# Kernel optimization log

Hardware: AMD Instinct MI355X
Metric: run time of the kernel (lower is better)

The kernel has to match this reference:

```python
import jax, jax.numpy as jnp
import numpy as np

N_NODES = 100000
N_EDGES = 1600000
N_GRAPHS = 1024
DIM_IN = 128
DIM_SF = 32
DIM_OUT = 8
EPS = 1e-5


def setup_inputs() -> dict:
    key = jax.random.key(0)
    ks = jax.random.split(key, 16)
    feat = jax.random.normal(ks[0], (N_NODES, DIM_IN), dtype=jnp.float32)
    self_feat = jax.random.normal(ks[1], (N_GRAPHS, DIM_SF), dtype=jnp.float32)
    src = jax.random.randint(ks[2], (N_EDGES,), 0, N_NODES)
    dst = jax.random.randint(ks[3], (N_EDGES,), 0, N_NODES)
    node2graph = jnp.sort(jax.random.randint(ks[4], (N_NODES,), 0, N_GRAPHS))

    def lin(k, din, dout):
        s = 1.0 / np.sqrt(din)
        kw, kb = jax.random.split(k)
        W = jax.random.uniform(kw, (din, dout), minval=-s, maxval=s, dtype=jnp.float32)
        b = jax.random.uniform(kb, (dout,), minval=-s, maxval=s, dtype=jnp.float32)
        return W, b

    W1, b1 = lin(ks[5], DIM_IN, 100)
    W2, b2 = lin(ks[6], 100, 20)
    Wf1, bf1 = lin(ks[7], 20 * DIM_SF, 128)
    Wf2, bf2 = lin(ks[8], 128, 32)
    Wf3, bf3 = lin(ks[9], 32, DIM_OUT)
    g1 = jnp.ones((128,), jnp.float32); be1 = jnp.zeros((128,), jnp.float32)
    g2 = jnp.ones((32,), jnp.float32); be2 = jnp.zeros((32,), jnp.float32)
    return dict(feat=feat, self_feat=self_feat, src=src, dst=dst,
                node2graph=node2graph, W1=W1, b1=b1, W2=W2, b2=b2,
                Wf1=Wf1, bf1=bf1, g1=g1, be1=be1,
                Wf2=Wf2, bf2=bf2, g2=g2, be2=be2, Wf3=Wf3, bf3=bf3)


def _gcn_layer(h, src, dst, W, b):
    # copy_u + mean reduce: segment-mean of source features onto destinations.
    n = h.shape[0]
    msum = jax.ops.segment_sum(h[src], dst, num_segments=n)        # [N, d]
    deg = jax.ops.segment_sum(jnp.ones((src.shape[0], 1), h.dtype), dst,
                              num_segments=n)                      # [N, 1]
    # DGL: nodes with no incoming messages keep their previous 'h'.
    agg = jnp.where(deg > 0, msum / jnp.maximum(deg, 1.0), h)
    return agg @ W + b


def _bn(x, gamma, beta):
    # BatchNorm1d in training mode: biased batch statistics.
    mu = jnp.mean(x, axis=0)
    var = jnp.mean((x - mu) ** 2, axis=0)
    return (x - mu) / jnp.sqrt(var + EPS) * gamma + beta


def reference(feat, self_feat, src, dst, node2graph,
              W1, b1, W2, b2, Wf1, bf1, g1, be1, Wf2, bf2, g2, be2, Wf3, bf3):
    h = jax.nn.relu(_gcn_layer(feat, src, dst, W1, b1))            # [N, 100]
    h = jax.nn.relu(_gcn_layer(h, src, dst, W2, b2))               # [N, 20]
    # dgl.mean_nodes: per-graph mean pooling
    hsum = jax.ops.segment_sum(h, node2graph, num_segments=N_GRAPHS)
    cnt = jax.ops.segment_sum(jnp.ones((h.shape[0], 1), h.dtype), node2graph,
                              num_segments=N_GRAPHS)
    hg = hsum / jnp.maximum(cnt, 1.0)                              # [G, 20]
    # Kronecker fusion: bmm(hg[:, :, None], self_feat[:, None, :])
    fused = (hg[:, :, None] * self_feat[:, None, :]).reshape(hg.shape[0], -1)
    out = jax.nn.relu(_bn(fused @ Wf1 + bf1, g1, be1))
    out = jax.nn.relu(_bn(out @ Wf2 + bf2, g2, be2))
    return out @ Wf3 + bf3                                         # [G, 8]
```

## Files before the change

kernel.cpp:

```cpp
#include <hip/hip_runtime.h>
#include <hip/hip_fp16.h>

#define N_NODES 100000
#define N_EDGES 1600000
#define N_GRAPHS 1024
#define DIM_IN 128
#define D1 100
#define D1P 128
#define D2 20
#define D2P 32
#define DIM_SF 32
#define DF1 128
#define DF2 32
#define DOUT 8
#define EPS 1e-5f
#define NPW 8

typedef _Float16 hh2 __attribute__((ext_vector_type(2)));

__device__ __forceinline__ void fdacc(unsigned u, float& lo, float& hi) {
  const hh2 MLO = {(_Float16)1.0f, (_Float16)0.0f};
  const hh2 MHI = {(_Float16)0.0f, (_Float16)1.0f};
  hh2 h = __builtin_bit_cast(hh2, u);
  lo = __builtin_amdgcn_fdot2(h, MLO, lo, false);
  hi = __builtin_amdgcn_fdot2(h, MHI, hi, false);
}

__device__ __forceinline__ unsigned pkadd(unsigned a, unsigned b) {
  __half2 x = __builtin_bit_cast(__half2, a);
  __half2 y = __builtin_bit_cast(__half2, b);
  return __builtin_bit_cast(unsigned, __hadd2(x, y));
}

#define NBK 512
#define BW 196
#define EPB 4096
#define NBLK1 ((N_EDGES + EPB - 1) / EPB)
#define GEMM1_NB (N_NODES / 80)

__global__ void __launch_bounds__(256) k_goff(const int* __restrict__ n2g,
                                              int* __restrict__ g_off,
                                              int* __restrict__ bucket_cnt) {
  int g = blockIdx.x * 256 + threadIdx.x;
  if (g < NBK) bucket_cnt[g] = 0;
  if (g > N_GRAPHS) return;
  if (g == N_GRAPHS) { g_off[g] = N_NODES; return; }
  int lo = 0, hi = N_NODES;
  while (lo < hi) {
    int mid = (lo + hi) >> 1;
    if (n2g[mid] < g) lo = mid + 1; else hi = mid;
  }
  g_off[g] = lo;
}

__global__ void __launch_bounds__(256) k_sc_gemm(const int* __restrict__ src,
                                                 const int* __restrict__ dst,
                                                 int* __restrict__ bucket_cnt,
                                                 unsigned* __restrict__ packed_out,
                                                 const float* __restrict__ feat,
                                                 const float* __restrict__ W1,
                                                 __half* __restrict__ p1h) {
  __shared__ __align__(16) char smem[DIM_IN * D1 * 4];
  int t = threadIdx.x;
  if (blockIdx.x < NBLK1) {
    int* hist   = (int*)smem;
    int* lbase  = (int*)(smem + 2048);
    int* gbase  = (int*)(smem + 4096);
    int* ssum   = (int*)(smem + 6144);
    unsigned* sval = (unsigned*)(smem + 7168);
    int* spos   = (int*)(smem + 23552);
    int blk = blockIdx.x;
    for (int i = t; i < NBK; i += 256) hist[i] = 0;
    __syncthreads();
    int base = blk * EPB;
    unsigned pk[16]; int bn[16]; int rk[16];
#pragma unroll
    for (int r = 0; r < 16; r++) {
      int e = base + r * 256 + t;
      bn[r] = -1;
      if (e < N_EDGES) {
        int dv = dst[e];
        unsigned b = (unsigned)dv / BW;
        unsigned ld = (unsigned)dv - b * BW;
        bn[r] = (int)b;
        pk[r] = ((unsigned)src[e] << 8) | ld;
        rk[r] = atomicAdd(&hist[b], 1);
      }
    }
    __syncthreads();
    int h0 = hist[2 * t], h1 = hist[2 * t + 1];
    int s = h0 + h1;
    ssum[t] = s; __syncthreads();
    for (int off = 1; off < 256; off <<= 1) {
      int x = (t >= off) ? ssum[t - off] : 0;
      __syncthreads();
      ssum[t] += x;
      __syncthreads();
    }
    int excl = ssum[t] - s;
    lbase[2 * t] = excl;
    lbase[2 * t + 1] = excl + h0;
    gbase[2 * t]     = (h0 > 0) ? (2 * t) * EPB     + atomicAdd(&bucket_cnt[2 * t],     h0) : 0;
    gbase[2 * t + 1] = (h1 > 0) ? (2 * t + 1) * EPB + atomicAdd(&bucket_cnt[2 * t + 1], h1) : 0;
    __syncthreads();
#pragma unroll
    for (int r = 0; r < 16; r++) {
      if (bn[r] >= 0) {
        int li = lbase[bn[r]] + rk[r];
        sval[li] = pk[r];
        spos[li] = gbase[bn[r]] + rk[r];
      }
    }
    __syncthreads();
    int cnt = N_EDGES - base; if (cnt > EPB) cnt = EPB;
    for (int i = t; i < cnt; i += 256) packed_out[spos[i]] = sval[i];
  } else {
    float* w1s = (float*)smem;
    for (int i = t; i < DIM_IN * D1; i += 256) w1s[i] = W1[i];
    __syncthreads();
    if (t >= 250) return;
    int q = t % 25, ng = t / 25;
    int n0 = (int)(blockIdx.x - NBLK1) * 80 + ng * 8;
    int c0 = q * 4;
    float acc[8][4] = {{0.f}};
    const float* f0 = feat + (size_t)n0 * DIM_IN;
    for (int k = 0; k < DIM_IN; k += 4) {
      float4 w0 = *(const float4*)&w1s[(k + 0) * D1 + c0];
      float4 w1 = *(const float4*)&w1s[(k + 1) * D1 + c0];
      float4 w2 = *(const float4*)&w1s[(k + 2) * D1 + c0];
      float4 w3 = *(const float4*)&w1s[(k + 3) * D1 + c0];
#pragma unroll
      for (int j = 0; j < 8; j++) {
        float4 f = *(const float4*)(f0 + j * DIM_IN + k);
        acc[j][0] += f.x * w0.x + f.y * w1.x + f.z * w2.x + f.w * w3.x;
        acc[j][1] += f.x * w0.y + f.y * w1.y + f.z * w2.y + f.w * w3.y;
        acc[j][2] += f.x * w0.z + f.y * w1.z + f.z * w2.z + f.w * w3.z;
        acc[j][3] += f.x * w0.w + f.y * w1.w + f.z * w2.w + f.w * w3.w;
      }
    }
#pragma unroll
    for (int j = 0; j < 8; j++) {
      __half2* d2 = (__half2*)(p1h + (size_t)(n0 + j) * D1P + c0);
      d2[0] = __floats2half2_rn(acc[j][0], acc[j][1]);
      d2[1] = __floats2half2_rn(acc[j][2], acc[j][3]);
    }
  }
}

__global__ void __launch_bounds__(256) k_bfine(const unsigned* __restrict__ packed_in,
                                               const int* __restrict__ bucket_cnt,
                                               int* __restrict__ csr,
                                               int* __restrict__ deg,
                                               int* __restrict__ row_off) {
  __shared__ unsigned sval[EPB];
  __shared__ int scsr[EPB];
  __shared__ int hist[256];
  __shared__ int soff[256];
  __shared__ int cur[256];
  int b = blockIdx.x, t = threadIdx.x;
  int start = b * EPB;
  int cnt = bucket_cnt[b];
  if (cnt > EPB) cnt = EPB;
  hist[t] = 0;
  __syncthreads();
  for (int i = t; i < cnt; i += 256) {
    unsigned v = packed_in[start + i];
    sval[i] = v;
    atomicAdd(&hist[v & 255u], 1);
  }
  __syncthreads();
  int h = hist[t];
  soff[t] = h; __syncthreads();
  for (int off = 1; off < 256; off <<= 1) {
    int x = (t >= off) ? soff[t - off] : 0;
    __syncthreads();
    soff[t] += x;
    __syncthreads();
  }
  int excl = soff[t] - h;
  cur[t] = excl;
  int n = b * BW + t;
  if (t < BW && n < N_NODES) { deg[n] = h; row_off[n] = start + excl; }
  __syncthreads();
  for (int i = t; i < cnt; i += 256) {
    unsigned v = sval[i];
    int pos = atomicAdd(&cur[v & 255u], 1);
    scsr[pos] = (int)(v >> 8);
  }
  __syncthreads();
  for (int i = t; i < cnt; i += 256) csr[start + i] = scsr[i];
}

__device__ __forceinline__ void acc8d(uint4 r, float4& A, float4& B) {
  fdacc(r.x, A.x, A.y);
  fdacc(r.y, A.z, A.w);
  fdacc(r.z, B.x, B.y);
  fdacc(r.w, B.z, B.w);
}

__global__ void __launch_bounds__(256) k_agg1(const __half* __restrict__ p1h,
                                              const int* __restrict__ deg,
                                              const int* __restrict__ row_off,
                                              const int* __restrict__ csr,
                                              const float* __restrict__ b1,
                                              const float* __restrict__ W2,
                                              __half* __restrict__ p2h) {
  __shared__ float w2s[D1 * D2];
  __shared__ float b1s[D1];
  __shared__ float hbuf[4][104];
  int t = threadIdx.x;
  for (int i = t; i < D1 * D2; i += 256) w2s[i] = W2[i];
  if (t < D1) b1s[t] = b1[t];
  __syncthreads();
  int w = t >> 6, lane = t & 63;
  int g = lane >> 4, o = lane & 15;
  const size_t oh = (size_t)(o * 8);
  int p = lane / 20;
  int j20 = lane - p * 20;
  int cbeg = (p == 0) ? 0 : (p == 1) ? 33 : 66;
  int cend = (p == 0) ? 33 : (p == 1) ? 66 : 100;
  if (p >= 3) { cbeg = 0; cend = 0; }
  int n0 = (blockIdx.x * 4 + w) * NPW;
  for (int nn = 0; nn < NPW; nn++) {
    int n = n0 + nn;
    int d = deg[n], ro = row_off[n];
    float4 A = {0.f, 0.f, 0.f, 0.f}, B = {0.f, 0.f, 0.f, 0.f};
    if (d > 0) {
      for (int base = 0; base < d; base += 64) {
        int m = d - base; if (m > 64) m = 64;
        int sv = (lane < m) ? csr[ro + base + lane] : 0;
        int nr = m >> 2;
        int r = 0;
        for (; r + 3 < nr; r += 4) {
          int sA = __shfl(sv, r * 4 + g);
          int sB = __shfl(sv, r * 4 + 4 + g);
          int sC = __shfl(sv, r * 4 + 8 + g);
          int sD = __shfl(sv, r * 4 + 12 + g);
          uint4 ra = *(const uint4*)(p1h + (size_t)sA * D1P + oh);
          uint4 rb = *(const uint4*)(p1h + (size_t)sB * D1P + oh);
          uint4 rc = *(const uint4*)(p1h + (size_t)sC * D1P + oh);
          uint4 rd = *(const uint4*)(p1h + (size_t)sD * D1P + oh);
          uint4 u, v2;
          u.x = pkadd(ra.x, rb.x); u.y = pkadd(ra.y, rb.y);
          u.z = pkadd(ra.z, rb.z); u.w = pkadd(ra.w, rb.w);
          v2.x = pkadd(rc.x, rd.x); v2.y = pkadd(rc.y, rd.y);
          v2.z = pkadd(rc.z, rd.z); v2.w = pkadd(rc.w, rd.w);
          acc8d(u, A, B);
          acc8d(v2, A, B);
        }
        if (r + 1 < nr) {
          int sA = __shfl(sv, r * 4 + g);
          int sB = __shfl(sv, r * 4 + 4 + g);
          uint4 ra = *(const uint4*)(p1h + (size_t)sA * D1P + oh);
          uint4 rb = *(const uint4*)(p1h + (size_t)sB * D1P + oh);
          uint4 u;
          u.x = pkadd(ra.x, rb.x); u.y = pkadd(ra.y, rb.y);
          u.z = pkadd(ra.z, rb.z); u.w = pkadd(ra.w, rb.w);
          acc8d(u, A, B);
          r += 2;
        }
        if (r < nr) {
          int sA = __shfl(sv, r * 4 + g);
          uint4 ra = *(const uint4*)(p1h + (size_t)sA * D1P + oh);
          acc8d(ra, A, B);
        }
        int rem = m & 3;
        int sT = __shfl(sv, nr * 4 + g);
        if (rem && g < rem) {
          uint4 ra = *(const uint4*)(p1h + (size_t)sT * D1P + oh);
          acc8d(ra, A, B);
        }
      }
    } else {
      if (g == 0) {
        uint4 ra = *(const uint4*)(p1h + (size_t)n * D1P + oh);
        acc8d(ra, A, B);
      }
    }
    float v[8] = {A.x, A.y, A.z, A.w, B.x, B.y, B.z, B.w};
#pragma unroll
    for (int j = 0; j < 8; j++) {
      v[j] += __shfl_down(v[j], 32);
      v[j] += __shfl_down(v[j], 16);
    }
    if (lane < 13) {
      float inv = (d > 0) ? 1.0f / (float)d : 1.0f;
#pragma unroll
      for (int j = 0; j < 8; j++) {
        int ch = 8 * lane + j;
        if (ch < D1) hbuf[w][ch] = fmaxf(v[j] * inv + b1s[ch], 0.f);
      }
    }
    float acc = 0.f;
    for (int c = cbeg; c < cend; c++) acc += hbuf[w][c] * w2s[c * D2 + j20];
    float t1 = __shfl_down(acc, 20);
    float t2 = __shfl_down(acc, 40);
    acc += t1 + t2;
    if (lane < D2)       p2h[(size_t)n * D2P + lane] = __float2half_rn(acc);
    else if (lane < D2P) p2h[(size_t)n * D2P + lane] = __float2half_rn(0.f);
  }
}

__global__ void __launch_bounds__(512) k_agg2(const __half* __restrict__ p2h,
                                              const int* __restrict__ deg,
                                              const int* __restrict__ row_off,
                                              const int* __restrict__ csr,
                                              const float* __restrict__ b2,
                                              const int* __restrict__ g_off,
                                              float* __restrict__ hg) {
  __shared__ float ssum[D2];
  __shared__ float b2s[D2];
  int t = threadIdx.x, w = t >> 6, lane = t & 63;
  int g = blockIdx.x;
  if (t < D2) { ssum[t] = 0.f; b2s[t] = b2[t]; }
  __syncthreads();
  const unsigned* pu = (const unsigned*)p2h;
  int n_lo = g_off[g], n_hi = g_off[g + 1];
  int nn = n_hi - n_lo;
  int e16 = lane >> 2, o = lane & 3;
  bool xtra = (o == 0);
  float4 GA = {0.f, 0.f, 0.f, 0.f};
  float4 GX = {0.f, 0.f, 0.f, 0.f};
  for (int n = n_lo + w; n < n_hi; n += 8) {
    int d = deg[n], ro = row_off[n];
    float4 A = {0.f, 0.f, 0.f, 0.f};
    float4 X = {0.f, 0.f, 0.f, 0.f};
    if (d > 0) {
      for (int base = 0; base < d; base += 64) {
        int m = d - base; if (m > 64) m = 64;
        int sv = (lane < m) ? csr[ro + base + lane] : 0;
        int nr = (m + 15) >> 4;
        for (int r = 0; r < nr; r++) {
          int ei = r * 16 + e16;
          int s0 = __shfl(sv, ei);
          if (ei < m) {
            const unsigned* row = pu + (size_t)s0 * 16;
            uint2 ra = *(const uint2*)(row + 2 * o);
            fdacc(ra.x, A.x, A.y);
            fdacc(ra.y, A.z, A.w);
            if (xtra) {
              uint2 rx = *(const uint2*)(row + 8);
              fdacc(rx.x, X.x, X.y);
              fdacc(rx.y, X.z, X.w);
            }
          }
        }
      }
    } else {
      if (e16 == 0) {
        const unsigned* row = pu + (size_t)n * 16;
        uint2 ra = *(const uint2*)(row + 2 * o);
        fdacc(ra.x, A.x, A.y);
        fdacc(ra.y, A.z, A.w);
        if (xtra) {
          uint2 rx = *(const uint2*)(row + 8);
          fdacc(rx.x, X.x, X.y);
          fdacc(rx.y, X.z, X.w);
        }
      }
    }
#pragma unroll
    for (int sft = 32; sft >= 4; sft >>= 1) {
      A.x += __shfl_down(A.x, sft); A.y += __shfl_down(A.y, sft);
      A.z += __shfl_down(A.z, sft); A.w += __shfl_down(A.w, sft);
      X.x += __shfl_down(X.x, sft); X.y += __shfl_down(X.y, sft);
      X.z += __shfl_down(X.z, sft); X.w += __shfl_down(X.w, sft);
    }
    float inv = (d > 0) ? 1.0f / (float)d : 1.0f;
    if (lane < 4) {
      int ch = 4 * lane;
      GA.x += fmaxf(A.x * inv + b2s[ch + 0], 0.f);
      GA.y += fmaxf(A.y * inv + b2s[ch + 1], 0.f);
      GA.z += fmaxf(A.z * inv + b2s[ch + 2], 0.f);
      GA.w += fmaxf(A.w * inv + b2s[ch + 3], 0.f);
      if (lane == 0) {
        GX.x += fmaxf(X.x * inv + b2s[16], 0.f);
        GX.y += fmaxf(X.y * inv + b2s[17], 0.f);
        GX.z += fmaxf(X.z * inv + b2s[18], 0.f);
        GX.w += fmaxf(X.w * inv + b2s[19], 0.f);
      }
    }
  }
  if (lane < 4) {
    int ch = 4 * lane;
    atomicAdd(&ssum[ch + 0], GA.x);
    atomicAdd(&ssum[ch + 1], GA.y);
    atomicAdd(&ssum[ch + 2], GA.z);
    atomicAdd(&ssum[ch + 3], GA.w);
    if (lane == 0) {
      atomicAdd(&ssum[16], GX.x);
      atomicAdd(&ssum[17], GX.y);
      atomicAdd(&ssum[18], GX.z);
      atomicAdd(&ssum[19], GX.w);
    }
  }
  __syncthreads();
  if (t < D2) {
    float inv = (nn > 0) ? 1.0f / (float)nn : 0.f;
    hg[g * D2 + t] = ssum[t] * inv;
  }
}

__global__ void __launch_bounds__(128) k_mlp1(const float* __restrict__ hg,
                                              const float* __restrict__ sf,
                                              const float* __restrict__ Wf1,
                                              const float* __restrict__ bf1,
                                              float* __restrict__ y1) {
  __shared__ float prod[D2 * DIM_SF];
  __shared__ float hgl[D2], sfl[DIM_SF];
  int g = blockIdx.x, t = threadIdx.x;
  if (t < D2) hgl[t] = hg[g * D2 + t];
  if (t < DIM_SF) sfl[t] = sf[g * DIM_SF + t];
  __syncthreads();
  for (int i = t; i < D2 * DIM_SF; i += 128) prod[i] = hgl[i >> 5] * sfl[i & 31];
  __syncthreads();
  float acc = bf1[t];
#pragma unroll 4
  for (int k = 0; k < D2 * DIM_SF; k++) acc += prod[k] * Wf1[k * DF1 + t];
  y1[g * DF1 + t] = acc;
}

__global__ void k_bnstats(const float* __restrict__ x, int ld,
                          float* __restrict__ mu, float* __restrict__ rstd) {
  __shared__ float ssum[256], ssq[256];
  int c = blockIdx.x, t = threadIdx.x;
  float s = 0.f, q = 0.f;
  for (int r = t; r < N_GRAPHS; r += 256) { float v = x[r * ld + c]; s += v; q += v * v; }
  ssum[t] = s; ssq[t] = q; __syncthreads();
  for (int off = 128; off > 0; off >>= 1) {
    if (t < off) { ssum[t] += ssum[t + off]; ssq[t] += ssq[t + off]; }
    __syncthreads();
  }
  if (t == 0) {
    float m = ssum[0] / (float)N_GRAPHS;
    float var = ssq[0] / (float)N_GRAPHS - m * m;
    mu[c] = m;
    rstd[c] = rsqrtf(var + EPS);
  }
}

__global__ void k_mlp2(const float* __restrict__ y1, const float* __restrict__ mu1,
                       const float* __restrict__ rstd1, const float* __restrict__ g1,
                       const float* __restrict__ be1, const float* __restrict__ Wf2,
                       const float* __restrict__ bf2, float* __restrict__ y2) {
  int idx = blockIdx.x * 256 + threadIdx.x;
  int g = idx >> 5, o = idx & 31;
  float acc = bf2[o];
  for (int k = 0; k < DF1; k++) {
    float x = (y1[g * DF1 + k] - mu1[k]) * rstd1[k] * g1[k] + be1[k];
    x = fmaxf(x, 0.f);
    acc += x * Wf2[k * DF2 + o];
  }
  y2[g * DF2 + o] = acc;
}

__global__ void k_mlp3(const float* __restrict__ y2, const float* __restrict__ mu2,
                       const float* __restrict__ rstd2, const float* __restrict__ g2,
                       const float* __restrict__ be2, const float* __restrict__ Wf3,
                       const float* __restrict__ bf3, float* __restrict__ out) {
  int idx = blockIdx.x * 256 + threadIdx.x;
  int g = idx >> 3, o = idx & 7;
  float acc = bf3[o];
  for (int k = 0; k < DF2; k++) {
    float x = (y2[g * DF2 + k] - mu2[k]) * rstd2[k] * g2[k] + be2[k];
    x = fmaxf(x, 0.f);
    acc += x * Wf3[k * DOUT + o];
  }
  out[g * DOUT + o] = acc;
}

extern "C" void kernel_launch(void* const* d_in, const int* in_sizes, int n_in,
                              void* d_out, int out_size, void* d_ws, size_t ws_size,
                              hipStream_t stream) {
  const float* feat = (const float*)d_in[0];
  const float* sf   = (const float*)d_in[1];
  const int*   src  = (const int*)d_in[2];
  const int*   dst  = (const int*)d_in[3];
  const int*   n2g  = (const int*)d_in[4];
  const float* W1   = (const float*)d_in[5];
  const float* b1   = (const float*)d_in[6];
  const float* W2   = (const float*)d_in[7];
  const float* b2   = (const float*)d_in[8];
  const float* Wf1  = (const float*)d_in[9];
  const float* bf1  = (const float*)d_in[10];
  const float* g1   = (const float*)d_in[11];
  const float* be1  = (const float*)d_in[12];
  const float* Wf2  = (const float*)d_in[13];
  const float* bf2  = (const float*)d_in[14];
  const float* g2   = (const float*)d_in[15];
  const float* be2  = (const float*)d_in[16];
  const float* Wf3  = (const float*)d_in[17];
  const float* bf3  = (const float*)d_in[18];
  float* out = (float*)d_out;

  char* ws = (char*)d_ws;
  size_t off = 0;
  auto alloc = [&](size_t bytes) -> void* {
    void* p = ws + off;
    off = (off + bytes + 255) & ~(size_t)255;
    return p;
  };
  int*      bucket_cnt = (int*)alloc(NBK * 4);
  int*      g_offs   = (int*)alloc((N_GRAPHS + 1) * 4);
  float*    hg       = (float*)alloc(N_GRAPHS * D2 * 4);
  int*      deg      = (int*)alloc(N_NODES * 4);
  int*      row_off  = (int*)alloc(N_NODES * 4);
  unsigned* packed   = (unsigned*)alloc((size_t)NBK * EPB * 4);
  int*      csr      = (int*)alloc((size_t)NBK * EPB * 4);
  __half*   p1h      = (__half*)alloc((size_t)N_NODES * D1P * 2);
  __half*   p2h      = (__half*)alloc((size_t)N_NODES * D2P * 2);
  float*    y1       = (float*)alloc((size_t)N_GRAPHS * DF1 * 4);
  float*    y2       = (float*)alloc((size_t)N_GRAPHS * DF2 * 4);
  float*    mu1      = (float*)alloc(DF1 * 4);
  float*    rstd1    = (float*)alloc(DF1 * 4);
  float*    mu2      = (float*)alloc(DF2 * 4);
  float*    rstd2    = (float*)alloc(DF2 * 4);

  k_goff<<<(N_GRAPHS + 1 + 255) / 256, 256, 0, stream>>>(n2g, g_offs, bucket_cnt);
  k_sc_gemm<<<NBLK1 + GEMM1_NB, 256, 0, stream>>>(src, dst, bucket_cnt, packed,
                                                  feat, W1, p1h);
  k_bfine<<<NBK, 256, 0, stream>>>(packed, bucket_cnt, csr, deg, row_off);
  k_agg1<<<N_NODES / (4 * NPW), 256, 0, stream>>>(p1h, deg, row_off, csr, b1, W2, p2h);
  k_agg2<<<N_GRAPHS, 512, 0, stream>>>(p2h, deg, row_off, csr, b2, g_offs, hg);
  k_mlp1<<<N_GRAPHS, 128, 0, stream>>>(hg, sf, Wf1, bf1, y1);
  k_bnstats<<<DF1, 256, 0, stream>>>(y1, DF1, mu1, rstd1);
  k_mlp2<<<(N_GRAPHS * DF2) / 256, 256, 0, stream>>>(y1, mu1, rstd1, g1, be1, Wf2, bf2, y2);
  k_bnstats<<<DF2, 256, 0, stream>>>(y2, DF2, mu2, rstd2);
  k_mlp3<<<(N_GRAPHS * DOUT) / 256, 256, 0, stream>>>(y2, mu2, rstd2, g2, be2, Wf3, bf3, out);
}
```

Measured before the change: 403.6 us.

## Fuse BN statistics into MLP kernels, simplify edge scatter, read W1 globally

Batch-norm statistics are now accumulated with atomics inside k_mlp1 and k_mlp2, which removes the two k_bnstats launches, and the stats buffer is zeroed in k_goff. The edge-bucketing pass drops its shared-memory prefix scan and staging, scattering packed edges straight to global memory. The GEMM1 path reads W1 from global memory instead of a 51 KB shared copy, which should raise occupancy, and NPW is halved for the aggregation kernel. The risks are uncoalesced scatter writes, float-atomic nondeterminism and variance computed as E[x^2]-mu^2.

```diff
diff --git a/kernel.cpp b/kernel.cpp
--- a/kernel.cpp
+++ b/kernel.cpp
@@ -14,7 +14,7 @@
 #define DF2 32
 #define DOUT 8
 #define EPS 1e-5f
-#define NPW 8
+#define NPW 4
 
 typedef _Float16 hh2 __attribute__((ext_vector_type(2)));
 
@@ -40,9 +40,9 @@
 
 __global__ void __launch_bounds__(256) k_goff(const int* __restrict__ n2g,
                                               int* __restrict__ g_off,
-                                              int* __restrict__ bucket_cnt) {
+                                              int* __restrict__ zero_base) {
   int g = blockIdx.x * 256 + threadIdx.x;
-  if (g < NBK) bucket_cnt[g] = 0;
+  if (g < NBK + 320) zero_base[g] = 0;
   if (g > N_GRAPHS) return;
   if (g == N_GRAPHS) { g_off[g] = N_NODES; return; }
   int lo = 0, hi = N_NODES;
@@ -60,15 +60,10 @@
                                                  const float* __restrict__ feat,
                                                  const float* __restrict__ W1,
                                                  __half* __restrict__ p1h) {
-  __shared__ __align__(16) char smem[DIM_IN * D1 * 4];
+  __shared__ int hist[NBK];
+  __shared__ int gbase[NBK];
   int t = threadIdx.x;
   if (blockIdx.x < NBLK1) {
-    int* hist   = (int*)smem;
-    int* lbase  = (int*)(smem + 2048);
-    int* gbase  = (int*)(smem + 4096);
-    int* ssum   = (int*)(smem + 6144);
-    unsigned* sval = (unsigned*)(smem + 7168);
-    int* spos   = (int*)(smem + 23552);
     int blk = blockIdx.x;
     for (int i = t; i < NBK; i += 256) hist[i] = 0;
     __syncthreads();
@@ -88,36 +83,16 @@
       }
     }
     __syncthreads();
-    int h0 = hist[2 * t], h1 = hist[2 * t + 1];
-    int s = h0 + h1;
-    ssum[t] = s; __syncthreads();
-    for (int off = 1; off < 256; off <<= 1) {
-      int x = (t >= off) ? ssum[t - off] : 0;
-      __syncthreads();
-      ssum[t] += x;
-      __syncthreads();
-    }
-    int excl = ssum[t] - s;
-    lbase[2 * t] = excl;
-    lbase[2 * t + 1] = excl + h0;
-    gbase[2 * t]     = (h0 > 0) ? (2 * t) * EPB     + atomicAdd(&bucket_cnt[2 * t],     h0) : 0;
-    gbase[2 * t + 1] = (h1 > 0) ? (2 * t + 1) * EPB + atomicAdd(&bucket_cnt[2 * t + 1], h1) : 0;
+    int b0 = 2 * t, b1 = 2 * t + 1;
+    int h0 = hist[b0], h1 = hist[b1];
+    gbase[b0] = (h0 > 0) ? b0 * EPB + atomicAdd(&bucket_cnt[b0], h0) : 0;
+    gbase[b1] = (h1 > 0) ? b1 * EPB + atomicAdd(&bucket_cnt[b1], h1) : 0;
     __syncthreads();
 #pragma unroll
     for (int r = 0; r < 16; r++) {
-      if (bn[r] >= 0) {
-        int li = lbase[bn[r]] + rk[r];
-        sval[li] = pk[r];
-        spos[li] = gbase[bn[r]] + rk[r];
-      }
-    }
-    __syncthreads();
-    int cnt = N_EDGES - base; if (cnt > EPB) cnt = EPB;
-    for (int i = t; i < cnt; i += 256) packed_out[spos[i]] = sval[i];
+      if (bn[r] >= 0) packed_out[gbase[bn[r]] + rk[r]] = pk[r];
+    }
   } else {
-    float* w1s = (float*)smem;
-    for (int i = t; i < DIM_IN * D1; i += 256) w1s[i] = W1[i];
-    __syncthreads();
     if (t >= 250) return;
     int q = t % 25, ng = t / 25;
     int n0 = (int)(blockIdx.x - NBLK1) * 80 + ng * 8;
@@ -125,10 +100,10 @@
     float acc[8][4] = {{0.f}};
     const float* f0 = feat + (size_t)n0 * DIM_IN;
     for (int k = 0; k < DIM_IN; k += 4) {
-      float4 w0 = *(const float4*)&w1s[(k + 0) * D1 + c0];
-      float4 w1 = *(const float4*)&w1s[(k + 1) * D1 + c0];
-      float4 w2 = *(const float4*)&w1s[(k + 2) * D1 + c0];
-      float4 w3 = *(const float4*)&w1s[(k + 3) * D1 + c0];
+      float4 w0 = *(const float4*)&W1[(k + 0) * D1 + c0];
+      float4 w1 = *(const float4*)&W1[(k + 1) * D1 + c0];
+      float4 w2 = *(const float4*)&W1[(k + 2) * D1 + c0];
+      float4 w3 = *(const float4*)&W1[(k + 3) * D1 + c0];
 #pragma unroll
       for (int j = 0; j < 8; j++) {
         float4 f = *(const float4*)(f0 + j * DIM_IN + k);
@@ -405,7 +380,8 @@
                                               const float* __restrict__ sf,
                                               const float* __restrict__ Wf1,
                                               const float* __restrict__ bf1,
-                                              float* __restrict__ y1) {
+                                              float* __restrict__ y1,
+                                              float* __restrict__ stats) {
   __shared__ float prod[D2 * DIM_SF];
   __shared__ float hgl[D2], sfl[DIM_SF];
   int g = blockIdx.x, t = threadIdx.x;
@@ -418,52 +394,71 @@
 #pragma unroll 4
   for (int k = 0; k < D2 * DIM_SF; k++) acc += prod[k] * Wf1[k * DF1 + t];
   y1[g * DF1 + t] = acc;
-}
-
-__global__ void k_bnstats(const float* __restrict__ x, int ld,
-                          float* __restrict__ mu, float* __restrict__ rstd) {
-  __shared__ float ssum[256], ssq[256];
-  int c = blockIdx.x, t = threadIdx.x;
-  float s = 0.f, q = 0.f;
-  for (int r = t; r < N_GRAPHS; r += 256) { float v = x[r * ld + c]; s += v; q += v * v; }
-  ssum[t] = s; ssq[t] = q; __syncthreads();
-  for (int off = 128; off > 0; off >>= 1) {
-    if (t < off) { ssum[t] += ssum[t + off]; ssq[t] += ssq[t + off]; }
-    __syncthreads();
-  }
-  if (t == 0) {
-    float m = ssum[0] / (float)N_GRAPHS;
-    float var = ssq[0] / (float)N_GRAPHS - m * m;
-    mu[c] = m;
-    rstd[c] = rsqrtf(var + EPS);
-  }
-}
-
-__global__ void k_mlp2(const float* __restrict__ y1, const float* __restrict__ mu1,
-                       const float* __restrict__ rstd1, const float* __restrict__ g1,
-                       const float* __restrict__ be1, const float* __restrict__ Wf2,
-                       const float* __restrict__ bf2, float* __restrict__ y2) {
-  int idx = blockIdx.x * 256 + threadIdx.x;
+  atomicAdd(&stats[t], acc);
+  atomicAdd(&stats[DF1 + t], acc * acc);
+}
+
+__global__ void __launch_bounds__(256) k_mlp2(const float* __restrict__ y1,
+                                              const float* __restrict__ stats,
+                                              const float* __restrict__ g1,
+                                              const float* __restrict__ be1,
+                                              const float* __restrict__ Wf2,
+                                              const float* __restrict__ bf2,
+                                              float* __restrict__ y2,
+                                              float* __restrict__ stats_out) {
+  __shared__ float nrm[DF1];
+  __shared__ float sh[DF1];
+  __shared__ float ps2[DF2], pq2[DF2];
+  int t = threadIdx.x;
+  if (t < DF1) {
+    float m = stats[t] * (1.0f / N_GRAPHS);
+    float var = stats[DF1 + t] * (1.0f / N_GRAPHS) - m * m;
+    float rs = rsqrtf(var + EPS);
+    nrm[t] = g1[t] * rs;
+    sh[t] = be1[t] - m * g1[t] * rs;
+  }
+  if (t < DF2) { ps2[t] = 0.f; pq2[t] = 0.f; }
+  __syncthreads();
+  int idx = blockIdx.x * 256 + t;
   int g = idx >> 5, o = idx & 31;
   float acc = bf2[o];
   for (int k = 0; k < DF1; k++) {
-    float x = (y1[g * DF1 + k] - mu1[k]) * rstd1[k] * g1[k] + be1[k];
-    x = fmaxf(x, 0.f);
+    float x = fmaxf(y1[g * DF1 + k] * nrm[k] + sh[k], 0.f);
     acc += x * Wf2[k * DF2 + o];
   }
   y2[g * DF2 + o] = acc;
-}
-
-__global__ void k_mlp3(const float* __restrict__ y2, const float* __restrict__ mu2,
-                       const float* __restrict__ rstd2, const float* __restrict__ g2,
-                       const float* __restrict__ be2, const float* __restrict__ Wf3,
-                       const float* __restrict__ bf3, float* __restrict__ out) {
-  int idx = blockIdx.x * 256 + threadIdx.x;
+  atomicAdd(&ps2[o], acc);
+  atomicAdd(&pq2[o], acc * acc);
+  __syncthreads();
+  if (t < DF2) {
+    atomicAdd((float*)&stats_out[256 + t], ps2[t]);
+    atomicAdd((float*)&stats_out[288 + t], pq2[t]);
+  }
+}
+
+__global__ void __launch_bounds__(256) k_mlp3(const float* __restrict__ y2,
+                                              const float* __restrict__ stats,
+                                              const float* __restrict__ g2,
+                                              const float* __restrict__ be2,
+                                              const float* __restrict__ Wf3,
+                                              const float* __restrict__ bf3,
+                                              float* __restrict__ out) {
+  __shared__ float nrm[DF2];
+  __shared__ float sh[DF2];
+  int t = threadIdx.x;
+  if (t < DF2) {
+    float m = stats[256 + t] * (1.0f / N_GRAPHS);
+    float var = stats[288 + t] * (1.0f / N_GRAPHS) - m * m;
+    float rs = rsqrtf(var + EPS);
+    nrm[t] = g2[t] * rs;
+    sh[t] = be2[t] - m * g2[t] * rs;
+  }
+  __syncthreads();
+  int idx = blockIdx.x * 256 + t;
   int g = idx >> 3, o = idx & 7;
   float acc = bf3[o];
   for (int k = 0; k < DF2; k++) {
-    float x = (y2[g * DF2 + k] - mu2[k]) * rstd2[k] * g2[k] + be2[k];
-    x = fmaxf(x, 0.f);
+    float x = fmaxf(y2[g * DF2 + k] * nrm[k] + sh[k], 0.f);
     acc += x * Wf3[k * DOUT + o];
   }
   out[g * DOUT + o] = acc;
@@ -501,6 +496,7 @@
     return p;
   };
   int*      bucket_cnt = (int*)alloc(NBK * 4);
+  float*    stats    = (float*)alloc(320 * 4);
   int*      g_offs   = (int*)alloc((N_GRAPHS + 1) * 4);
   float*    hg       = (float*)alloc(N_GRAPHS * D2 * 4);
   int*      deg      = (int*)alloc(N_NODES * 4);
@@ -511,10 +507,6 @@
   __half*   p2h      = (__half*)alloc((size_t)N_NODES * D2P * 2);
   float*    y1       = (float*)alloc((size_t)N_GRAPHS * DF1 * 4);
   float*    y2       = (float*)alloc((size_t)N_GRAPHS * DF2 * 4);
-  float*    mu1      = (float*)alloc(DF1 * 4);
-  float*    rstd1    = (float*)alloc(DF1 * 4);
-  float*    mu2      = (float*)alloc(DF2 * 4);
-  float*    rstd2    = (float*)alloc(DF2 * 4);
 
   k_goff<<<(N_GRAPHS + 1 + 255) / 256, 256, 0, stream>>>(n2g, g_offs, bucket_cnt);
   k_sc_gemm<<<NBLK1 + GEMM1_NB, 256, 0, stream>>>(src, dst, bucket_cnt, packed,
@@ -522,9 +514,7 @@
   k_bfine<<<NBK, 256, 0, stream>>>(packed, bucket_cnt, csr, deg, row_off);
   k_agg1<<<N_NODES / (4 * NPW), 256, 0, stream>>>(p1h, deg, row_off, csr, b1, W2, p2h);
   k_agg2<<<N_GRAPHS, 512, 0, stream>>>(p2h, deg, row_off, csr, b2, g_offs, hg);
-  k_mlp1<<<N_GRAPHS, 128, 0, stream>>>(hg, sf, Wf1, bf1, y1);
-  k_bnstats<<<DF1, 256, 0, stream>>>(y1, DF1, mu1, rstd1);
-  k_mlp2<<<(N_GRAPHS * DF2) / 256, 256, 0, stream>>>(y1, mu1, rstd1, g1, be1, Wf2, bf2, y2);
-  k_bnstats<<<DF2, 256, 0, stream>>>(y2, DF2, mu2, rstd2);
-  k_mlp3<<<(N_GRAPHS * DOUT) / 256, 256, 0, stream>>>(y2, mu2, rstd2, g2, be2, Wf3, bf3, out);
-}
+  k_mlp1<<<N_GRAPHS, 128, 0, stream>>>(hg, sf, Wf1, bf1, y1, stats);
+  k_mlp2<<<(N_GRAPHS * DF2) / 256, 256, 0, stream>>>(y1, stats, g1, be1, Wf2, bf2, y2, stats);
+  k_mlp3<<<(N_GRAPHS * DOUT) / 256, 256, 0, stream>>>(y2, stats, g2, be2, Wf3, bf3, out);
+}
```

New measurement: 467.6 us. +15.9%, slower.
